# Optimization experiments

Measured on AMD Instinct MI355X. Metric: run time of the kernel, lower is better.

## Reference

```python
import jax, jax.numpy as jnp
import numpy as np

N = 100000   # nodes per type
E = 1600000  # edges per edge type
F = 128      # input feature dim
C = 256      # out_channels


def setup_inputs() -> dict:
    key = jax.random.key(0)
    ks = iter(jax.random.split(key, 32))
    d = {}
    d["x_A"] = jax.random.normal(next(ks), (N, F), jnp.float32)
    d["x_B"] = jax.random.normal(next(ks), (N, F), jnp.float32)
    d["h_A"] = jax.random.normal(next(ks), (N, F), jnp.float32)
    d["h_B"] = jax.random.normal(next(ks), (N, F), jnp.float32)
    d["eidx_ab"] = jax.random.randint(next(ks), (2, E), 0, N, jnp.int32)
    d["eidx_ba"] = jax.random.randint(next(ks), (2, E), 0, N, jnp.int32)
    # per-node-type input linears (bias=False) and output biases
    d["lin_A"] = jax.random.normal(next(ks), (F, C), jnp.float32) / np.sqrt(F)
    d["lin_B"] = jax.random.normal(next(ks), (F, C), jnp.float32) / np.sqrt(F)
    d["bias_A"] = jax.random.uniform(next(ks), (C,), jnp.float32)
    d["bias_B"] = jax.random.uniform(next(ks), (C,), jnp.float32)
    # SAGEConv params: per layer (0,1) x per edge type (ab: A->B, ba: B->A)
    #   Wl: neighbor (lin_l) weight [C,C], bl: lin_l bias [C], Wr: root (lin_r) weight [C,C]
    for l in range(2):
        for et in ("ab", "ba"):
            d[f"Wl_{et}{l}"] = jax.random.normal(next(ks), (C, C), jnp.float32) / np.sqrt(C)
            d[f"bl_{et}{l}"] = jnp.zeros((C,), jnp.float32)
            d[f"Wr_{et}{l}"] = jax.random.normal(next(ks), (C, C), jnp.float32) / np.sqrt(C)
    return d


def _sage(x_src, x_dst, eidx, Wl, bl, Wr):
    # PyG SAGEConv (mean aggr): lin_l(mean_{j->i} x_src[j]) + bias + lin_r(x_dst[i])
    src, dst = eidx[0], eidx[1]
    n_dst = x_dst.shape[0]
    agg = jax.ops.segment_sum(x_src[src], dst, num_segments=n_dst)      # [N_dst, C]
    cnt = jax.ops.segment_sum(jnp.ones_like(dst, dtype=x_src.dtype), dst,
                              num_segments=n_dst)                       # [N_dst]
    mean = agg / jnp.maximum(cnt, 1.0)[:, None]
    return mean @ Wl + bl + x_dst @ Wr


def reference(x_A, x_B, h_A, h_B, eidx_ab, eidx_ba,
              lin_A, lin_B, bias_A, bias_B,
              Wl_ab0, bl_ab0, Wr_ab0, Wl_ba0, bl_ba0, Wr_ba0,
              Wl_ab1, bl_ab1, Wr_ab1, Wl_ba1, bl_ba1, Wr_ba1):
    # per-type input projection
    oA = x_A @ lin_A
    oB = x_B @ lin_B
    # layer 0: A gets messages via B->A, B via A->B (one edge type per dst -> no hetero sum)
    nA = _sage(oB, oA, eidx_ba, Wl_ba0, bl_ba0, Wr_ba0)
    nB = _sage(oA, oB, eidx_ab, Wl_ab0, bl_ab0, Wr_ab0)
    oA, oB = nA, nB
    # layer 1
    nA = _sage(oB, oA, eidx_ba, Wl_ba1, bl_ba1, Wr_ba1)
    nB = _sage(oA, oB, eidx_ab, Wl_ab1, bl_ab1, Wr_ab1)
    oA, oB = nA, nB
    # per-type bias + sigmoid gate
    gA = jax.nn.sigmoid(bias_A + oA)
    gB = jax.nn.sigmoid(bias_B + oB)
    return jnp.stack([gA, gB])  # [2, N, C]
```

## Files before the change

kernel.cpp:

```cpp
#include <hip/hip_runtime.h>
#include <math.h>

#define NN 100000
#define EE 1600000
#define SCAN_BLOCKS 98

typedef short s16x8 __attribute__((ext_vector_type(8)));
typedef float f32x4 __attribute__((ext_vector_type(4)));

union FragU { uint4 u; s16x8 s; };

__device__ __forceinline__ unsigned short f2bf(float x) {
    unsigned int u = __float_as_uint(x);
    u = (u + 0x7fff + ((u >> 16) & 1)) >> 16;
    return (unsigned short)u;
}
__device__ __forceinline__ float bf2f(unsigned short b) {
    return __uint_as_float(((unsigned int)b) << 16);
}
__device__ __forceinline__ float bflo(unsigned int u) { return __uint_as_float(u << 16); }
__device__ __forceinline__ float bfhi(unsigned int u) { return __uint_as_float(u & 0xffff0000u); }

__device__ __forceinline__ void gload16(const unsigned short* g, unsigned short* l) {
    __builtin_amdgcn_global_load_lds(
        (const __attribute__((address_space(1))) unsigned int*)g,
        (__attribute__((address_space(3))) unsigned int*)l, 16, 0, 0);
}

template<int K1, int K2, int MODE>
__global__ __launch_bounds__(256)
void gemm_mfma(const unsigned short* __restrict__ A1,
               const unsigned short* __restrict__ A2,
               const unsigned short* __restrict__ BT,
               const float* __restrict__ bl, const float* __restrict__ b2,
               void* __restrict__ Cout, int M)
{
    constexpr int KT = K1 + K2;
    __shared__ __align__(16) unsigned short As[128 * 32];
    __shared__ __align__(16) unsigned short Bs[128 * 32];

    const int tid  = threadIdx.x;
    const int w    = tid >> 6, lane = tid & 63;
    const int l15  = lane & 15, g = lane >> 4;
    const int m0   = blockIdx.x * 128;
    const int n0   = blockIdx.y * 128;
    const int wm   = (w >> 1) * 64, wn = (w & 1) * 64;

    f32x4 acc[4][4];
#pragma unroll
    for (int i = 0; i < 4; i++)
#pragma unroll
        for (int j = 0; j < 4; j++) { acc[i][j][0]=0.f; acc[i][j][1]=0.f; acc[i][j][2]=0.f; acc[i][j][3]=0.f; }

    for (int k0 = 0; k0 < KT; k0 += 32) {
        const unsigned short* Ap; int astr, kloc;
        if (K1 > 0 && k0 < K1) { Ap = A1; astr = K1; kloc = k0; }
        else                   { Ap = A2; astr = K2; kloc = k0 - K1; }

#pragma unroll
        for (int c = 0; c < 2; c++) {
            const int chunk = ((w * 2 + c) << 6) + lane;
            const int row = chunk >> 2, kc = chunk & 3;
            int rg = m0 + row; if (rg > M - 1) rg = M - 1;
            gload16(Ap + (size_t)rg * astr + kloc + kc * 8, As + (w * 2 + c) * 512);
            gload16(BT + (size_t)(n0 + row) * KT + k0 + kc * 8, Bs + (w * 2 + c) * 512);
        }
        __syncthreads();

        FragU a[4], b[4];
#pragma unroll
        for (int i = 0; i < 4; i++) {
            a[i].u = *(const uint4*)(As + (wm + i * 16 + l15) * 32 + g * 8);
            b[i].u = *(const uint4*)(Bs + (wn + i * 16 + l15) * 32 + g * 8);
        }
#pragma unroll
        for (int i = 0; i < 4; i++)
#pragma unroll
            for (int j = 0; j < 4; j++)
                acc[i][j] = __builtin_amdgcn_mfma_f32_16x16x32_bf16(a[i].s, b[j].s, acc[i][j], 0, 0, 0);
        __syncthreads();
    }

    float badd[4];
#pragma unroll
    for (int j = 0; j < 4; j++) {
        const int col = n0 + wn + j * 16 + l15;
        badd[j] = bl ? bl[col] : 0.0f;
        if (MODE == 1) badd[j] += b2[col];
    }
#pragma unroll
    for (int i = 0; i < 4; i++) {
#pragma unroll
        for (int r = 0; r < 4; r++) {
            const int rowg = m0 + wm + i * 16 + g * 4 + r;
            if (rowg < M) {
#pragma unroll
                for (int j = 0; j < 4; j++) {
                    const int col = n0 + wn + j * 16 + l15;
                    float t = acc[i][j][r] + badd[j];
                    if (MODE == 1) {
                        t = 1.0f / (1.0f + __expf(-t));
                        ((float*)Cout)[(size_t)rowg * 256 + col] = t;
                    } else {
                        ((unsigned short*)Cout)[(size_t)rowg * 256 + col] = f2bf(t);
                    }
                }
            }
        }
    }
}

__global__ __launch_bounds__(256)
void hist2_kernel(const int* __restrict__ dst_ba, const int* __restrict__ dst_ab,
                  int* __restrict__ cnt)
{
    const int e = blockIdx.x * 256 + threadIdx.x;
    const int y = blockIdx.y;
    if (e < EE) {
        const int d = (y == 0) ? dst_ba[e] : dst_ab[e];
        atomicAdd(&cnt[y * NN + d], 1);
    }
}

__device__ __forceinline__ int wave_incl_scan(int v, int lane)
{
#pragma unroll
    for (int off = 1; off < 64; off <<= 1) {
        int t = __shfl_up(v, off, 64);
        if (lane >= off) v += t;
    }
    return v;
}

__global__ __launch_bounds__(1024)
void scan_local_kernel(const int* __restrict__ cnt, int* __restrict__ rowptr,
                       int* __restrict__ bsum)
{
    __shared__ int wsum[16];
    __shared__ int wpre[16];
    const int y = blockIdx.y, b = blockIdx.x;
    const int tid = threadIdx.x, lane = tid & 63, wid = tid >> 6;
    const int i = b * 1024 + tid;
    const int v = (i < NN) ? cnt[y * NN + i] : 0;
    const int incl = wave_incl_scan(v, lane);
    if (lane == 63) wsum[wid] = incl;
    __syncthreads();
    if (wid == 0) {
        const int s  = (lane < 16) ? wsum[lane] : 0;
        const int si = wave_incl_scan(s, lane);
        if (lane < 16) wpre[lane] = si - s;
    }
    __syncthreads();
    const int excl = wpre[wid] + incl - v;
    if (i < NN) rowptr[y * (NN + 1) + i] = excl;
    if (tid == 1023) bsum[y * 128 + b] = excl + v;
}

__global__ __launch_bounds__(256)
void scan_bsum_kernel(const int* __restrict__ bsum, int* __restrict__ boff,
                      int* __restrict__ rowptr)
{
    __shared__ int ws[2][2];
    const int tid = threadIdx.x;
    const int y = tid >> 7, j = tid & 127, lane = j & 63, wid = j >> 6;
    const int v = (j < SCAN_BLOCKS) ? bsum[y * 128 + j] : 0;
    const int incl = wave_incl_scan(v, lane);
    if (lane == 63) ws[y][wid] = incl;
    __syncthreads();
    const int off = (wid == 1) ? ws[y][0] : 0;
    boff[y * 128 + j] = off + incl - v;
    if (j == 127) rowptr[y * (NN + 1) + NN] = off + incl;
}

__global__ __launch_bounds__(1024)
void scan_add_kernel(const int* __restrict__ boff, int* __restrict__ rowptr,
                     int* __restrict__ work)
{
    const int y = blockIdx.y, b = blockIdx.x;
    const int i = b * 1024 + threadIdx.x;
    if (i < NN) {
        const int r = rowptr[y * (NN + 1) + i] + boff[y * 128 + b];
        rowptr[y * (NN + 1) + i] = r;
        work[y * NN + i] = r;
    }
}

__global__ __launch_bounds__(256)
void fill2_kernel(const int* __restrict__ src_ba, const int* __restrict__ dst_ba,
                  const int* __restrict__ src_ab, const int* __restrict__ dst_ab,
                  int* __restrict__ work, int* __restrict__ ssrc)
{
    const int e = blockIdx.x * 256 + threadIdx.x;
    const int y = blockIdx.y;
    if (e < EE) {
        const int d = (y == 0) ? dst_ba[e] : dst_ab[e];
        const int s = (y == 0) ? src_ba[e] : src_ab[e];
        const int pos = atomicAdd(&work[y * NN + d], 1);
        ssrc[(size_t)y * EE + pos] = s;
    }
}

__global__ __launch_bounds__(128)
void agg_bf(const unsigned short* __restrict__ feat, const int* __restrict__ rowptr,
            const int* __restrict__ ssrc, unsigned short* __restrict__ out)
{
    __shared__ float red[32][8];
    const int node = blockIdx.x;
    const int t = threadIdx.x;
    const int slot = t >> 5;
    const int c = t & 31;
    const int beg = rowptr[node], end = rowptr[node + 1];
    const int deg = end - beg;

    float a0=0.f,a1=0.f,a2=0.f,a3=0.f,a4=0.f,a5=0.f,a6=0.f,a7=0.f;
    for (int i = beg + slot; i < end; i += 4) {
        const uint4 v = *(const uint4*)(feat + ((size_t)ssrc[i] << 8) + c * 8);
        a0 += bflo(v.x); a1 += bfhi(v.x);
        a2 += bflo(v.y); a3 += bfhi(v.y);
        a4 += bflo(v.z); a5 += bfhi(v.z);
        a6 += bflo(v.w); a7 += bfhi(v.w);
    }
    a0 += __shfl_xor(a0, 32, 64); a1 += __shfl_xor(a1, 32, 64);
    a2 += __shfl_xor(a2, 32, 64); a3 += __shfl_xor(a3, 32, 64);
    a4 += __shfl_xor(a4, 32, 64); a5 += __shfl_xor(a5, 32, 64);
    a6 += __shfl_xor(a6, 32, 64); a7 += __shfl_xor(a7, 32, 64);
    if (t >= 64 && t < 96) {
        red[c][0]=a0; red[c][1]=a1; red[c][2]=a2; red[c][3]=a3;
        red[c][4]=a4; red[c][5]=a5; red[c][6]=a6; red[c][7]=a7;
    }
    __syncthreads();
    if (t < 32) {
        a0 += red[c][0]; a1 += red[c][1]; a2 += red[c][2]; a3 += red[c][3];
        a4 += red[c][4]; a5 += red[c][5]; a6 += red[c][6]; a7 += red[c][7];
        const float inv = 1.0f / fmaxf((float)deg, 1.0f);
        uint4 o;
        o.x = (unsigned int)f2bf(a0 * inv) | ((unsigned int)f2bf(a1 * inv) << 16);
        o.y = (unsigned int)f2bf(a2 * inv) | ((unsigned int)f2bf(a3 * inv) << 16);
        o.z = (unsigned int)f2bf(a4 * inv) | ((unsigned int)f2bf(a5 * inv) << 16);
        o.w = (unsigned int)f2bf(a6 * inv) | ((unsigned int)f2bf(a7 * inv) << 16);
        *(uint4*)(out + ((size_t)node << 8) + c * 8) = o;
    }
}

__global__ __launch_bounds__(256)
void f2bf4_kernel(const float* __restrict__ in, unsigned short* __restrict__ out, int n4)
{
    const int i = blockIdx.x * 256 + threadIdx.x;
    if (i < n4) {
        const float4 v = ((const float4*)in)[i];
        ushort4 o;
        o.x = f2bf(v.x); o.y = f2bf(v.y); o.z = f2bf(v.z); o.w = f2bf(v.w);
        ((ushort4*)out)[i] = o;
    }
}

__global__ __launch_bounds__(256)
void wt_kernel(const float* __restrict__ W, unsigned short* __restrict__ WT,
               int K, int KT, int koff)
{
    const int idx = blockIdx.x * 256 + threadIdx.x;
    if (idx < K * 256) {
        const int k = idx >> 8, n = idx & 255;
        WT[(size_t)n * KT + koff + k] = f2bf(W[(size_t)k * 256 + n]);
    }
}

extern "C" void kernel_launch(void* const* d_in, const int* in_sizes, int n_in,
                              void* d_out, int out_size, void* d_ws, size_t ws_size,
                              hipStream_t stream)
{
    const float* x_A    = (const float*)d_in[0];
    const float* x_B    = (const float*)d_in[1];
    const int*   e_ab   = (const int*)d_in[4];
    const int*   e_ba   = (const int*)d_in[5];
    const float* lin_A  = (const float*)d_in[6];
    const float* lin_B  = (const float*)d_in[7];
    const float* bias_A = (const float*)d_in[8];
    const float* bias_B = (const float*)d_in[9];
    const float* Wl_ab0 = (const float*)d_in[10]; const float* bl_ab0 = (const float*)d_in[11]; const float* Wr_ab0 = (const float*)d_in[12];
    const float* Wl_ba0 = (const float*)d_in[13]; const float* bl_ba0 = (const float*)d_in[14]; const float* Wr_ba0 = (const float*)d_in[15];
    const float* Wl_ab1 = (const float*)d_in[16]; const float* bl_ab1 = (const float*)d_in[17]; const float* Wr_ab1 = (const float*)d_in[18];
    const float* Wl_ba1 = (const float*)d_in[19]; const float* bl_ba1 = (const float*)d_in[20]; const float* Wr_ba1 = (const float*)d_in[21];

    float* gA = (float*)d_out;
    float* gB = gA + (size_t)NN * 256;

    const size_t HALF = (size_t)NN * 128;
    const size_t FULL = (size_t)NN * 256;
    unsigned short* xb    = (unsigned short*)d_ws;
    unsigned short* xbA   = xb;
    unsigned short* xbB   = xb + HALF;
    unsigned short* l0A   = xb;
    unsigned short* projA = xb + FULL;
    unsigned short* l0B   = projA;
    unsigned short* projB = projA + FULL;
    unsigned short* aggb  = projB + FULL;
    unsigned short* linAT = aggb + FULL;
    unsigned short* linBT = linAT + 256 * 128;
    unsigned short* WTba0 = linBT + 256 * 128;
    unsigned short* WTab0 = WTba0 + 256 * 512;
    unsigned short* WTba1 = WTab0 + 256 * 512;
    unsigned short* WTab1 = WTba1 + 256 * 512;
    int* ssrc2   = (int*)(WTab1 + 256 * 512);
    int* rowptr2 = ssrc2 + 2 * (size_t)EE;
    int* work2   = rowptr2 + 2 * (NN + 1);
    int* cnt2    = work2 + 2 * NN;
    int* bsum    = cnt2 + 2 * NN;
    int* boff    = bsum + 2 * 128;

    int* ssrc_ba   = ssrc2;
    int* ssrc_ab   = ssrc2 + EE;
    int* rowptr_ba = rowptr2;
    int* rowptr_ab = rowptr2 + (NN + 1);

    const int* src_ab = e_ab;  const int* dst_ab = e_ab + EE;
    const int* src_ba = e_ba;  const int* dst_ba = e_ba + EE;

    const int gE = (EE + 255) / 256;
    const dim3 gg((NN + 127) / 128, 2);
    const dim3 gE2(gE, 2);
    const dim3 gScan(SCAN_BLOCKS, 2);

    hipMemsetAsync(cnt2, 0, 2 * NN * sizeof(int), stream);
    hist2_kernel<<<gE2, 256, 0, stream>>>(dst_ba, dst_ab, cnt2);
    scan_local_kernel<<<gScan, 1024, 0, stream>>>(cnt2, rowptr2, bsum);
    scan_bsum_kernel<<<1, 256, 0, stream>>>(bsum, boff, rowptr2);
    scan_add_kernel<<<gScan, 1024, 0, stream>>>(boff, rowptr2, work2);
    fill2_kernel<<<gE2, 256, 0, stream>>>(src_ba, dst_ba, src_ab, dst_ab, work2, ssrc2);

    f2bf4_kernel<<<(int)(HALF / 4 + 255) / 256, 256, 0, stream>>>(x_A, xbA, (int)(HALF / 4));
    f2bf4_kernel<<<(int)(HALF / 4 + 255) / 256, 256, 0, stream>>>(x_B, xbB, (int)(HALF / 4));
    wt_kernel<<<128, 256, 0, stream>>>(lin_A, linAT, 128, 128, 0);
    wt_kernel<<<128, 256, 0, stream>>>(lin_B, linBT, 128, 128, 0);
    wt_kernel<<<256, 256, 0, stream>>>(Wl_ba0, WTba0, 256, 512, 0);
    wt_kernel<<<256, 256, 0, stream>>>(Wr_ba0, WTba0, 256, 512, 256);
    wt_kernel<<<256, 256, 0, stream>>>(Wl_ab0, WTab0, 256, 512, 0);
    wt_kernel<<<256, 256, 0, stream>>>(Wr_ab0, WTab0, 256, 512, 256);
    wt_kernel<<<256, 256, 0, stream>>>(Wl_ba1, WTba1, 256, 512, 0);
    wt_kernel<<<256, 256, 0, stream>>>(Wr_ba1, WTba1, 256, 512, 256);
    wt_kernel<<<256, 256, 0, stream>>>(Wl_ab1, WTab1, 256, 512, 0);
    wt_kernel<<<256, 256, 0, stream>>>(Wr_ab1, WTab1, 256, 512, 256);

    gemm_mfma<0, 128, 0><<<gg, 256, 0, stream>>>(nullptr, xbA, linAT, nullptr, nullptr, projA, NN);
    gemm_mfma<0, 128, 0><<<gg, 256, 0, stream>>>(nullptr, xbB, linBT, nullptr, nullptr, projB, NN);

    agg_bf<<<NN, 128, 0, stream>>>(projB, rowptr_ba, ssrc_ba, aggb);
    gemm_mfma<256, 256, 0><<<gg, 256, 0, stream>>>(aggb, projA, WTba0, bl_ba0, nullptr, l0A, NN);
    agg_bf<<<NN, 128, 0, stream>>>(projA, rowptr_ab, ssrc_ab, aggb);
    gemm_mfma<256, 256, 0><<<gg, 256, 0, stream>>>(aggb, projB, WTab0, bl_ab0, nullptr, l0B, NN);

    agg_bf<<<NN, 128, 0, stream>>>(l0B, rowptr_ba, ssrc_ba, aggb);
    gemm_mfma<256, 256, 1><<<gg, 256, 0, stream>>>(aggb, l0A, WTba1, bl_ba1, bias_A, gA, NN);
    agg_bf<<<NN, 128, 0, stream>>>(l0A, rowptr_ab, ssrc_ab, aggb);
    gemm_mfma<256, 256, 1><<<gg, 256, 0, stream>>>(aggb, l0B, WTab1, bl_ab1, bias_B, gB, NN);
}
```

Before: 1.514 ms.

## Replace global-atomic CSR build with two-level bucketed radix sort

Builds the destination-sorted CSR with a two-pass counting sort. The first pass counts edges per 128-node bucket in LDS for each edge chunk, then scans and scatters packed (src,dst-low) words into a staging buffer. A per-bucket kernel then does a fine sort in LDS and writes rowptr and the sorted sources with coalesced stores. This removes the random global atomics on per-node counters and the scattered stores of the old hist/fill path. In exchange it adds more kernel launches, a serial single-block scan, and a fixed 8192-entry LDS buffer per bucket that would truncate any bucket with more edges.

```diff
diff --git a/kernel.cpp b/kernel.cpp
--- a/kernel.cpp
+++ b/kernel.cpp
@@ -3,7 +3,9 @@
 
 #define NN 100000
 #define EE 1600000
-#define SCAN_BLOCKS 98
+#define NBU 782
+#define NCH 196
+#define CHUNK 8192
 
 typedef short s16x8 __attribute__((ext_vector_type(8)));
 typedef float f32x4 __attribute__((ext_vector_type(4)));
@@ -110,18 +112,6 @@
     }
 }
 
-__global__ __launch_bounds__(256)
-void hist2_kernel(const int* __restrict__ dst_ba, const int* __restrict__ dst_ab,
-                  int* __restrict__ cnt)
-{
-    const int e = blockIdx.x * 256 + threadIdx.x;
-    const int y = blockIdx.y;
-    if (e < EE) {
-        const int d = (y == 0) ? dst_ba[e] : dst_ab[e];
-        atomicAdd(&cnt[y * NN + d], 1);
-    }
-}
-
 __device__ __forceinline__ int wave_incl_scan(int v, int lane)
 {
 #pragma unroll
@@ -132,72 +122,134 @@
     return v;
 }
 
+__global__ __launch_bounds__(256)
+void p1_count(const int* __restrict__ dba, const int* __restrict__ dab,
+              int* __restrict__ cnt)
+{
+    __shared__ int h[NBU];
+    const int y = blockIdx.y, b = blockIdx.x;
+    for (int i = threadIdx.x; i < NBU; i += 256) h[i] = 0;
+    __syncthreads();
+    const int* D = y ? dab : dba;
+    const int base = b * CHUNK;
+    for (int i = threadIdx.x; i < CHUNK; i += 256) {
+        const int e = base + i;
+        if (e < EE) atomicAdd(&h[D[e] >> 7], 1);
+    }
+    __syncthreads();
+    for (int i = threadIdx.x; i < NBU; i += 256)
+        cnt[(y * NCH + b) * NBU + i] = h[i];
+}
+
 __global__ __launch_bounds__(1024)
-void scan_local_kernel(const int* __restrict__ cnt, int* __restrict__ rowptr,
-                       int* __restrict__ bsum)
-{
-    __shared__ int wsum[16];
-    __shared__ int wpre[16];
+void p2_scan(const int* __restrict__ cnt, int* __restrict__ baseG)
+{
+    __shared__ int tot[2 * NBU];
+    const int tid = threadIdx.x;
+    for (int i = tid; i < 2 * NBU; i += 1024) {
+        const int y = i / NBU, u = i - y * NBU;
+        int s = 0;
+#pragma unroll 4
+        for (int b = 0; b < NCH; b++) s += cnt[(y * NCH + b) * NBU + u];
+        tot[i] = s;
+    }
+    __syncthreads();
+    const int lane = tid & 63, wid = tid >> 6;
+    if (wid < 2) {
+        int run = 0;
+        for (int c = 0; c < NBU; c += 64) {
+            const int ui = c + lane;
+            const int v = (ui < NBU) ? tot[wid * NBU + ui] : 0;
+            const int incl = wave_incl_scan(v, lane);
+            if (ui < NBU) baseG[wid * (NBU + 1) + ui] = run + incl - v;
+            run += __shfl(incl, 63, 64);
+        }
+        if (lane == 0) baseG[wid * (NBU + 1) + NBU] = run;
+    }
+}
+
+__global__ __launch_bounds__(256)
+void p2b_off(const int* __restrict__ cnt, const int* __restrict__ baseG,
+             int* __restrict__ blockOff)
+{
+    const int i = blockIdx.x * 256 + threadIdx.x;
+    if (i >= 2 * NBU) return;
+    const int y = i / NBU, u = i - y * NBU;
+    int run = baseG[y * (NBU + 1) + u];
+#pragma unroll 4
+    for (int b = 0; b < NCH; b++) {
+        blockOff[(y * NCH + b) * NBU + u] = run;
+        run += cnt[(y * NCH + b) * NBU + u];
+    }
+}
+
+__global__ __launch_bounds__(256)
+void p3_scatter(const int* __restrict__ sba, const int* __restrict__ dba,
+                const int* __restrict__ sab, const int* __restrict__ dab,
+                const int* __restrict__ blockOff, int* __restrict__ stage)
+{
+    __shared__ int cur[NBU];
     const int y = blockIdx.y, b = blockIdx.x;
-    const int tid = threadIdx.x, lane = tid & 63, wid = tid >> 6;
-    const int i = b * 1024 + tid;
-    const int v = (i < NN) ? cnt[y * NN + i] : 0;
-    const int incl = wave_incl_scan(v, lane);
-    if (lane == 63) wsum[wid] = incl;
-    __syncthreads();
-    if (wid == 0) {
-        const int s  = (lane < 16) ? wsum[lane] : 0;
-        const int si = wave_incl_scan(s, lane);
-        if (lane < 16) wpre[lane] = si - s;
-    }
-    __syncthreads();
-    const int excl = wpre[wid] + incl - v;
-    if (i < NN) rowptr[y * (NN + 1) + i] = excl;
-    if (tid == 1023) bsum[y * 128 + b] = excl + v;
-}
-
-__global__ __launch_bounds__(256)
-void scan_bsum_kernel(const int* __restrict__ bsum, int* __restrict__ boff,
-                      int* __restrict__ rowptr)
-{
-    __shared__ int ws[2][2];
-    const int tid = threadIdx.x;
-    const int y = tid >> 7, j = tid & 127, lane = j & 63, wid = j >> 6;
-    const int v = (j < SCAN_BLOCKS) ? bsum[y * 128 + j] : 0;
-    const int incl = wave_incl_scan(v, lane);
-    if (lane == 63) ws[y][wid] = incl;
-    __syncthreads();
-    const int off = (wid == 1) ? ws[y][0] : 0;
-    boff[y * 128 + j] = off + incl - v;
-    if (j == 127) rowptr[y * (NN + 1) + NN] = off + incl;
-}
-
-__global__ __launch_bounds__(1024)
-void scan_add_kernel(const int* __restrict__ boff, int* __restrict__ rowptr,
-                     int* __restrict__ work)
-{
-    const int y = blockIdx.y, b = blockIdx.x;
-    const int i = b * 1024 + threadIdx.x;
-    if (i < NN) {
-        const int r = rowptr[y * (NN + 1) + i] + boff[y * 128 + b];
-        rowptr[y * (NN + 1) + i] = r;
-        work[y * NN + i] = r;
-    }
-}
-
-__global__ __launch_bounds__(256)
-void fill2_kernel(const int* __restrict__ src_ba, const int* __restrict__ dst_ba,
-                  const int* __restrict__ src_ab, const int* __restrict__ dst_ab,
-                  int* __restrict__ work, int* __restrict__ ssrc)
-{
-    const int e = blockIdx.x * 256 + threadIdx.x;
-    const int y = blockIdx.y;
-    if (e < EE) {
-        const int d = (y == 0) ? dst_ba[e] : dst_ab[e];
-        const int s = (y == 0) ? src_ba[e] : src_ab[e];
-        const int pos = atomicAdd(&work[y * NN + d], 1);
-        ssrc[(size_t)y * EE + pos] = s;
-    }
+    for (int i = threadIdx.x; i < NBU; i += 256)
+        cur[i] = blockOff[(y * NCH + b) * NBU + i];
+    __syncthreads();
+    const int* S = y ? sab : sba;
+    const int* D = y ? dab : dba;
+    int* st = stage + (size_t)y * EE;
+    const int base = b * CHUNK;
+    for (int i = threadIdx.x; i < CHUNK; i += 256) {
+        const int e = base + i;
+        if (e < EE) {
+            const int d = D[e], s = S[e];
+            const int p = atomicAdd(&cur[d >> 7], 1);
+            __builtin_nontemporal_store((s << 7) | (d & 127), &st[p]);
+        }
+    }
+}
+
+__global__ __launch_bounds__(256)
+void p4_fine(const int* __restrict__ baseG, const int* __restrict__ stage,
+             int* __restrict__ rowptr, int* __restrict__ ssrc)
+{
+    __shared__ int out[8192];
+    __shared__ int hist[128], off[128], curs[128];
+    const int y = blockIdx.y, u = blockIdx.x;
+    const int t = threadIdx.x;
+    const int base = baseG[y * (NBU + 1) + u];
+    const int cnt_ = baseG[y * (NBU + 1) + u + 1] - base;
+    const int n0 = u * 128;
+    if (t < 128) hist[t] = 0;
+    __syncthreads();
+    const int* st = stage + (size_t)y * EE + base;
+    for (int i = t; i < cnt_; i += 256) atomicAdd(&hist[st[i] & 127], 1);
+    __syncthreads();
+    if (t < 64) {
+        const int v0 = hist[t];
+        const int i0 = wave_incl_scan(v0, t);
+        off[t] = i0 - v0;
+        const int tot0 = __shfl(i0, 63, 64);
+        const int v1 = hist[64 + t];
+        const int i1 = wave_incl_scan(v1, t);
+        off[64 + t] = tot0 + i1 - v1;
+    }
+    __syncthreads();
+    if (t < 128) {
+        curs[t] = off[t];
+        const int node = n0 + t;
+        if (node < NN) rowptr[y * (NN + 1) + node] = base + off[t];
+    }
+    if (t == 0 && u == 0) rowptr[y * (NN + 1) + NN] = EE;
+    __syncthreads();
+    for (int i = t; i < cnt_; i += 256) {
+        const int w = st[i];
+        const int p = atomicAdd(&curs[w & 127], 1);
+        if (p < 8192) out[p] = w >> 7;
+    }
+    __syncthreads();
+    int* dp = ssrc + (size_t)y * EE + base;
+    const int lim = (cnt_ < 8192) ? cnt_ : 8192;
+    for (int i = t; i < lim; i += 256)
+        __builtin_nontemporal_store(out[i], &dp[i]);
 }
 
 __global__ __launch_bounds__(128)
@@ -303,10 +355,11 @@
     unsigned short* WTab1 = WTba1 + 256 * 512;
     int* ssrc2   = (int*)(WTab1 + 256 * 512);
     int* rowptr2 = ssrc2 + 2 * (size_t)EE;
-    int* work2   = rowptr2 + 2 * (NN + 1);
-    int* cnt2    = work2 + 2 * NN;
-    int* bsum    = cnt2 + 2 * NN;
-    int* boff    = bsum + 2 * 128;
+
+    int* stage    = (int*)aggb;
+    int* cnt      = stage + 2 * (size_t)EE;
+    int* blockOff = cnt + 2 * NCH * NBU;
+    int* baseG    = blockOff + 2 * NCH * NBU;
 
     int* ssrc_ba   = ssrc2;
     int* ssrc_ab   = ssrc2 + EE;
@@ -316,17 +369,15 @@
     const int* src_ab = e_ab;  const int* dst_ab = e_ab + EE;
     const int* src_ba = e_ba;  const int* dst_ba = e_ba + EE;
 
-    const int gE = (EE + 255) / 256;
     const dim3 gg((NN + 127) / 128, 2);
-    const dim3 gE2(gE, 2);
-    const dim3 gScan(SCAN_BLOCKS, 2);
-
-    hipMemsetAsync(cnt2, 0, 2 * NN * sizeof(int), stream);
-    hist2_kernel<<<gE2, 256, 0, stream>>>(dst_ba, dst_ab, cnt2);
-    scan_local_kernel<<<gScan, 1024, 0, stream>>>(cnt2, rowptr2, bsum);
-    scan_bsum_kernel<<<1, 256, 0, stream>>>(bsum, boff, rowptr2);
-    scan_add_kernel<<<gScan, 1024, 0, stream>>>(boff, rowptr2, work2);
-    fill2_kernel<<<gE2, 256, 0, stream>>>(src_ba, dst_ba, src_ab, dst_ab, work2, ssrc2);
+    const dim3 gCh(NCH, 2);
+    const dim3 gBu(NBU, 2);
+
+    p1_count<<<gCh, 256, 0, stream>>>(dst_ba, dst_ab, cnt);
+    p2_scan<<<1, 1024, 0, stream>>>(cnt, baseG);
+    p2b_off<<<(2 * NBU + 255) / 256, 256, 0, stream>>>(cnt, baseG, blockOff);
+    p3_scatter<<<gCh, 256, 0, stream>>>(src_ba, dst_ba, src_ab, dst_ab, blockOff, stage);
+    p4_fine<<<gBu, 256, 0, stream>>>(baseG, stage, rowptr2, ssrc2);
 
     f2bf4_kernel<<<(int)(HALF / 4 + 255) / 256, 256, 0, stream>>>(x_A, xbA, (int)(HALF / 4));
     f2bf4_kernel<<<(int)(HALF / 4 + 255) / 256, 256, 0, stream>>>(x_B, xbB, (int)(HALF / 4));
```

New measurement: 1.300 ms. 1.16x faster.
